# Kernel optimization log

Measured on AMD Instinct MI355X. Metric: run time of the kernel, lower is better.

Reference implementation:

```python
import jax, jax.numpy as jnp
import numpy as np

B, T, C, H = 4, 4096, 512, 64  # batch, seq(patches), n_embed, head_size

def setup_inputs() -> dict:
    key = jax.random.key(0)
    kx, kk, kq, kv = jax.random.split(key, 4)
    x = jax.random.normal(kx, (B, T, C), dtype=jnp.float32)
    # torch nn.Linear(n_embed, head_size).weight is [H, C]; store transposed [C, H]
    Wk = jax.random.normal(kk, (C, H), dtype=jnp.float32) / np.sqrt(C)
    Wq = jax.random.normal(kq, (C, H), dtype=jnp.float32) / np.sqrt(C)
    Wv = jax.random.normal(kv, (C, H), dtype=jnp.float32) / np.sqrt(C)
    return {"x": x, "Wk": Wk, "Wq": Wq, "Wv": Wv}

def reference(x, Wk, Wq, Wv):
    Bn, Tn, Cn = x.shape
    k = x @ Wk  # [B,T,H]
    q = x @ Wq
    v = x @ Wv
    # NOTE: original scales by C**-0.5 with C = n_embed (input dim), not head_size
    scores = jnp.einsum('bth,bsh->bts', q, k) * (Cn ** -0.5)  # [B,T,T]
    causal = jnp.tril(jnp.ones((Tn, Tn), dtype=bool))
    scores = jnp.where(causal, scores, -jnp.inf)
    attn = jax.nn.softmax(scores, axis=-1)
    return jnp.einsum('bts,bsh->bth', attn, v)  # [B,T,H]
```

## Files before the change

### kernel.cpp

```cpp
#include <hip/hip_runtime.h>
#include <hip/hip_bf16.h>

#define Bb 4
#define Tt 4096

typedef __bf16 bf16;
typedef __attribute__((ext_vector_type(8))) __bf16 bf16x8;
typedef __attribute__((ext_vector_type(4))) __bf16 bf16x4;
typedef __attribute__((ext_vector_type(4))) float f32x4;


__global__ __launch_bounds__(256) void wt_kernel(const float* __restrict__ Wk,
                                                 const float* __restrict__ Wq,
                                                 const float* __restrict__ Wv,
                                                 bf16* __restrict__ wt) {
  int idx = blockIdx.x * 256 + threadIdx.x;
  int mat = idx >> 15;
  int rem = idx & 32767;
  int n = rem >> 9;
  int k = rem & 511;
  const float* W = (mat == 0) ? Wk : (mat == 1) ? Wq : Wv;
  float v = W[k * 64 + n];
  if (mat == 1) v *= 0.044194173824159216f;
  wt[idx] = (bf16)v;
}

__global__ __launch_bounds__(256) void proj_kernel(const float* __restrict__ x,
                                                   const bf16* __restrict__ wt,
                                                   bf16* __restrict__ Kb,
                                                   bf16* __restrict__ Qb,
                                                   bf16* __restrict__ VTb) {
  __shared__ __attribute__((aligned(16))) bf16 xs[16][520];
  int tid = threadIdx.x;
  int row0 = blockIdx.x * 16;

  int sr = tid >> 4, sc = (tid & 15) * 4;
  const float* xr = x + (size_t)(row0 + sr) * 512;
#pragma unroll
  for (int j = 0; j < 8; ++j) {
    f32x4 a = *(const f32x4*)(xr + sc + j * 64);
    bf16x4 h;
#pragma unroll
    for (int e = 0; e < 4; ++e) h[e] = (bf16)a[e];
    *(bf16x4*)&xs[sr][sc + j * 64] = h;
  }
  __syncthreads();

  int wave = tid >> 6, lane = tid & 63, m = lane & 15, quad = lane >> 4;
  f32x4 acc[3];
#pragma unroll
  for (int i = 0; i < 3; ++i) acc[i] = (f32x4){0.f, 0.f, 0.f, 0.f};

#pragma unroll 4
  for (int kk = 0; kk < 512; kk += 32) {
    bf16x8 af = *(const bf16x8*)&xs[m][kk + quad * 8];
#pragma unroll
    for (int i = 0; i < 3; ++i) {
      int nt = wave * 3 + i;
      bf16x8 bfr = *(const bf16x8*)(wt + (nt >> 2) * 32768 +
                                    (((nt & 3) * 16) + m) * 512 + kk + quad * 8);
      acc[i] = __builtin_amdgcn_mfma_f32_16x16x32_bf16(af, bfr, acc[i], 0, 0, 0);
    }
  }

  int b = row0 >> 12, tloc = row0 & 4095;
#pragma unroll
  for (int i = 0; i < 3; ++i) {
    int nt = wave * 3 + i, mat = nt >> 2, n0 = (nt & 3) * 16;
    if (mat == 2) {
      bf16x4 pv;
#pragma unroll
      for (int r = 0; r < 4; ++r) pv[r] = (bf16)acc[i][r];
      *(bf16x4*)&VTb[((size_t)b * 64 + n0 + m) * 4096 + tloc + quad * 4] = pv;
    } else {
      bf16* dst = (mat == 0) ? Kb : Qb;
#pragma unroll
      for (int r = 0; r < 4; ++r)
        dst[(size_t)(row0 + quad * 4 + r) * 64 + n0 + m] = (bf16)acc[i][r];
    }
  }
}

__global__ __launch_bounds__(256) void attn_kernel(const bf16* __restrict__ Qb,
                                                   const bf16* __restrict__ Kb,
                                                   const bf16* __restrict__ VTb,
                                                   bf16* __restrict__ Opart,
                                                   float* __restrict__ Lpart,
                                                   float* __restrict__ out) {
  __shared__ __attribute__((aligned(16))) bf16 Kt[64][72];
  __shared__ __attribute__((aligned(16))) bf16 Vt[64][72];
  __shared__ __attribute__((aligned(16))) bf16 Pl[4][16][72];

  int tid = threadIdx.x, wave = tid >> 6, lane = tid & 63;
  int m = lane & 15, quad = lane >> 4, kq = quad * 8;

  int uu = 1151 - (int)blockIdx.x;
  int b = uu / 288, u2 = uu % 288;
  int g = 0;
  while (u2 >= 4 * (g + 1) * (g + 2)) ++g;
  int rr = u2 - 4 * g * (g + 1);
  int qi = 8 * g + rr / (g + 1);
  int c = rr % (g + 1);
  int t0 = qi * 64;
  int s_beg = c * 512;
  int s_end = min(s_beg + 512, t0 + 64);
  int niter = (s_end - s_beg) >> 6;

  const bf16* Qp = Qb + ((size_t)b * Tt + t0 + wave * 16 + m) * 64;
  bf16x8 aq0 = *(const bf16x8*)(Qp + kq);
  bf16x8 aq1 = *(const bf16x8*)(Qp + 32 + kq);

  bf16x8 onesb;
#pragma unroll
  for (int j = 0; j < 8; ++j) onesb[j] = (bf16)1.0f;

  f32x4 o[4];
#pragma unroll
  for (int i = 0; i < 4; ++i) o[i] = (f32x4){0.f, 0.f, 0.f, 0.f};
  f32x4 lsum = (f32x4){0.f, 0.f, 0.f, 0.f};

  int r_ = tid >> 2, seg = tid & 3;
  const bf16* Kbase = Kb + (size_t)b * Tt * 64;
  const bf16* VTbase = VTb + (size_t)b * 64 * 4096;

  const bf16* ks = Kbase + (size_t)(s_beg + r_) * 64 + seg * 16;
  bf16x8 k0 = *(const bf16x8*)ks;
  bf16x8 k1 = *(const bf16x8*)(ks + 8);
  const bf16* vs = VTbase + (size_t)r_ * 4096 + s_beg + seg * 16;
  bf16x8 v0 = *(const bf16x8*)vs;
  bf16x8 v1 = *(const bf16x8*)(vs + 8);

  for (int i = 0; i < niter; ++i) {
    int s0 = s_beg + i * 64;
    __syncthreads();
    *(bf16x8*)&Kt[r_][seg * 16] = k0;
    *(bf16x8*)&Kt[r_][seg * 16 + 8] = k1;
    *(bf16x8*)&Vt[r_][seg * 16] = v0;
    *(bf16x8*)&Vt[r_][seg * 16 + 8] = v1;
    __syncthreads();
    if (i + 1 < niter) {
      int sn = s0 + 64;
      const bf16* ks2 = Kbase + (size_t)(sn + r_) * 64 + seg * 16;
      k0 = *(const bf16x8*)ks2;
      k1 = *(const bf16x8*)(ks2 + 8);
      const bf16* vs2 = VTbase + (size_t)r_ * 4096 + sn + seg * 16;
      v0 = *(const bf16x8*)vs2;
      v1 = *(const bf16x8*)(vs2 + 8);
    }

    f32x4 s[4];
#pragma unroll
    for (int nt = 0; nt < 4; ++nt) {
      bf16x8 b0 = *(const bf16x8*)&Kt[nt * 16 + m][kq];
      bf16x8 b1 = *(const bf16x8*)&Kt[nt * 16 + m][32 + kq];
      f32x4 sa = (f32x4){0.f, 0.f, 0.f, 0.f};
      sa = __builtin_amdgcn_mfma_f32_16x16x32_bf16(aq0, b0, sa, 0, 0, 0);
      sa = __builtin_amdgcn_mfma_f32_16x16x32_bf16(aq1, b1, sa, 0, 0, 0);
      s[nt] = sa;
    }

    if (s0 + 64 > t0) {
#pragma unroll
      for (int nt = 0; nt < 4; ++nt) {
        int col = s0 + nt * 16 + m;
#pragma unroll
        for (int r = 0; r < 4; ++r) {
          int row = t0 + wave * 16 + quad * 4 + r;
          if (col > row) s[nt][r] = -1e30f;
        }
      }
    }

#pragma unroll
    for (int nt = 0; nt < 4; ++nt)
#pragma unroll
      for (int r = 0; r < 4; ++r)
        Pl[wave][quad * 4 + r][nt * 16 + m] = (bf16)__expf(s[nt][r]);

#pragma unroll
    for (int ch = 0; ch < 2; ++ch) {
      bf16x8 ap = *(const bf16x8*)&Pl[wave][m][ch * 32 + kq];
      lsum = __builtin_amdgcn_mfma_f32_16x16x32_bf16(ap, onesb, lsum, 0, 0, 0);
#pragma unroll
      for (int nt = 0; nt < 4; ++nt) {
        bf16x8 bv = *(const bf16x8*)&Vt[nt * 16 + m][ch * 32 + kq];
        o[nt] = __builtin_amdgcn_mfma_f32_16x16x32_bf16(ap, bv, o[nt], 0, 0, 0);
      }
    }
  }

  int rl0 = wave * 16 + quad * 4;
  if (qi < 8) {
    float* op = out + ((size_t)b * Tt + t0) * 64;
#pragma unroll
    for (int r = 0; r < 4; ++r) {
      float inv = 1.0f / lsum[r];
#pragma unroll
      for (int nt = 0; nt < 4; ++nt)
        op[(size_t)(rl0 + r) * 64 + nt * 16 + m] = o[nt][r] * inv;
    }
  } else {
    int p = b * 288 + 4 * g * (g + 1) + (qi - 8 * g) * (g + 1) + c;
    bf16* Op = Opart + (size_t)p * 4096;
#pragma unroll
    for (int r = 0; r < 4; ++r)
#pragma unroll
      for (int nt = 0; nt < 4; ++nt)
        Op[(rl0 + r) * 64 + nt * 16 + m] = (bf16)o[nt][r];
    if (m == 0) {
#pragma unroll
      for (int r = 0; r < 4; ++r) Lpart[p * 64 + rl0 + r] = lsum[r];
    }
  }
}

__global__ __launch_bounds__(256) void combine_kernel(const bf16* __restrict__ Opart,
                                                      const float* __restrict__ Lpart,
                                                      float* __restrict__ out) {
  int blk = blockIdx.x;
  int b = blk / 224, rem = blk % 224;
  int qi = 8 + (rem >> 2), rq = rem & 3;
  int g = qi >> 3, nc = g + 1;
  int pb = b * 288 + 4 * g * (g + 1) + (qi - 8 * g) * (g + 1);
  int t = threadIdx.x, col = t & 63, rl = t >> 6;
#pragma unroll
  for (int rr = 0; rr < 4; ++rr) {
    int row64 = rq * 16 + rl * 4 + rr;
    float L = 0.f, acc = 0.f;
    for (int cc = 0; cc < nc; ++cc) {
      L += Lpart[(pb + cc) * 64 + row64];
      acc += (float)Opart[(size_t)(pb + cc) * 4096 + row64 * 64 + col];
    }
    out[((size_t)b * Tt + qi * 64 + row64) * 64 + col] = acc / L;
  }
}

extern "C" void kernel_launch(void* const* d_in, const int* in_sizes, int n_in,
                              void* d_out, int out_size, void* d_ws, size_t ws_size,
                              hipStream_t stream) {
  const float* x = (const float*)d_in[0];
  const float* Wk = (const float*)d_in[1];
  const float* Wq = (const float*)d_in[2];
  const float* Wv = (const float*)d_in[3];
  float* out = (float*)d_out;

  char* w = (char*)d_ws;
  bf16* wt = (bf16*)w;
  bf16* Kb = (bf16*)(w + 196608);
  bf16* Qb = (bf16*)(w + 2293760);
  bf16* VTb = (bf16*)(w + 4390912);
  bf16* Opart = (bf16*)(w + 6488064);
  float* Lpart = (float*)(w + 15925248);

  wt_kernel<<<384, 256, 0, stream>>>(Wk, Wq, Wv, wt);
  proj_kernel<<<1024, 256, 0, stream>>>(x, wt, Kb, Qb, VTb);
  attn_kernel<<<1152, 256, 0, stream>>>(Qb, Kb, VTb, Opart, Lpart, out);
  combine_kernel<<<896, 256, 0, stream>>>(Opart, Lpart, out);
}
```

Baseline: 137.0 us.

## Keep P in registers via permlane swap, double-buffer K/V, use exp2

Computes S transposed (K as the A operand) so each lane holds probabilities that permlane16_swap can rearrange into the MFMA A-operand layout. This removes the per-wave LDS round trip for P. K/V tiles are double-buffered in shared memory, leaving one barrier per iteration instead of two, and exp is replaced by hardware exp2 with log2(e) folded into the Q scale. Occupancy is hinted with launch_bounds(256,4). The costs are more LDS per block and a more intricate column permutation when indexing V.

```diff
diff --git a/kernel.cpp b/kernel.cpp
--- a/kernel.cpp
+++ b/kernel.cpp
@@ -7,7 +7,10 @@
 typedef __bf16 bf16;
 typedef __attribute__((ext_vector_type(8))) __bf16 bf16x8;
 typedef __attribute__((ext_vector_type(4))) __bf16 bf16x4;
+typedef __attribute__((ext_vector_type(2))) __bf16 bf16x2;
 typedef __attribute__((ext_vector_type(4))) float f32x4;
+typedef __attribute__((ext_vector_type(2))) unsigned int u32x2;
+typedef __attribute__((ext_vector_type(4))) unsigned int u32x4;
 
 
 __global__ __launch_bounds__(256) void wt_kernel(const float* __restrict__ Wk,
@@ -21,7 +24,7 @@
   int k = rem & 511;
   const float* W = (mat == 0) ? Wk : (mat == 1) ? Wq : Wv;
   float v = W[k * 64 + n];
-  if (mat == 1) v *= 0.044194173824159216f;
+  if (mat == 1) v *= 0.0637587165f;
   wt[idx] = (bf16)v;
 }
 
@@ -81,15 +84,26 @@
   }
 }
 
-__global__ __launch_bounds__(256) void attn_kernel(const bf16* __restrict__ Qb,
-                                                   const bf16* __restrict__ Kb,
-                                                   const bf16* __restrict__ VTb,
-                                                   bf16* __restrict__ Opart,
-                                                   float* __restrict__ Lpart,
-                                                   float* __restrict__ out) {
-  __shared__ __attribute__((aligned(16))) bf16 Kt[64][72];
-  __shared__ __attribute__((aligned(16))) bf16 Vt[64][72];
-  __shared__ __attribute__((aligned(16))) bf16 Pl[4][16][72];
+static __device__ inline unsigned pk2(float lo, float hi) {
+  bf16x2 t;
+  t[0] = (bf16)lo;
+  t[1] = (bf16)hi;
+  return __builtin_bit_cast(unsigned int, t);
+}
+static __device__ inline void plswap(unsigned& a, unsigned& b) {
+  u32x2 r = __builtin_amdgcn_permlane16_swap(a, b, false, false);
+  a = r.x;
+  b = r.y;
+}
+
+__global__ __launch_bounds__(256, 4) void attn_kernel(const bf16* __restrict__ Qb,
+                                                      const bf16* __restrict__ Kb,
+                                                      const bf16* __restrict__ VTb,
+                                                      bf16* __restrict__ Opart,
+                                                      float* __restrict__ Lpart,
+                                                      float* __restrict__ out) {
+  __shared__ __attribute__((aligned(16))) bf16 Kt[2][64][72];
+  __shared__ __attribute__((aligned(16))) bf16 Vt[2][64][72];
 
   int tid = threadIdx.x, wave = tid >> 6, lane = tid & 63;
   int m = lane & 15, quad = lane >> 4, kq = quad * 8;
@@ -123,22 +137,29 @@
   const bf16* Kbase = Kb + (size_t)b * Tt * 64;
   const bf16* VTbase = VTb + (size_t)b * 64 * 4096;
 
-  const bf16* ks = Kbase + (size_t)(s_beg + r_) * 64 + seg * 16;
-  bf16x8 k0 = *(const bf16x8*)ks;
-  bf16x8 k1 = *(const bf16x8*)(ks + 8);
-  const bf16* vs = VTbase + (size_t)r_ * 4096 + s_beg + seg * 16;
-  bf16x8 v0 = *(const bf16x8*)vs;
-  bf16x8 v1 = *(const bf16x8*)(vs + 8);
+  {
+    const bf16* ks = Kbase + (size_t)(s_beg + r_) * 64 + seg * 16;
+    bf16x8 k0 = *(const bf16x8*)ks;
+    bf16x8 k1 = *(const bf16x8*)(ks + 8);
+    const bf16* vs = VTbase + (size_t)r_ * 4096 + s_beg + seg * 16;
+    bf16x8 v0 = *(const bf16x8*)vs;
+    bf16x8 v1 = *(const bf16x8*)(vs + 8);
+    *(bf16x8*)&Kt[0][r_][seg * 16] = k0;
+    *(bf16x8*)&Kt[0][r_][seg * 16 + 8] = k1;
+    *(bf16x8*)&Vt[0][r_][seg * 16] = v0;
+    *(bf16x8*)&Vt[0][r_][seg * 16 + 8] = v1;
+  }
+  __syncthreads();
+
+  int qrow = t0 + wave * 16 + m;
 
   for (int i = 0; i < niter; ++i) {
     int s0 = s_beg + i * 64;
-    __syncthreads();
-    *(bf16x8*)&Kt[r_][seg * 16] = k0;
-    *(bf16x8*)&Kt[r_][seg * 16 + 8] = k1;
-    *(bf16x8*)&Vt[r_][seg * 16] = v0;
-    *(bf16x8*)&Vt[r_][seg * 16 + 8] = v1;
-    __syncthreads();
-    if (i + 1 < niter) {
+    int cb = i & 1;
+    bool more = (i + 1 < niter);
+
+    bf16x8 k0, k1, v0, v1;
+    if (more) {
       int sn = s0 + 64;
       const bf16* ks2 = Kbase + (size_t)(sn + r_) * 64 + seg * 16;
       k0 = *(const bf16x8*)ks2;
@@ -151,41 +172,58 @@
     f32x4 s[4];
 #pragma unroll
     for (int nt = 0; nt < 4; ++nt) {
-      bf16x8 b0 = *(const bf16x8*)&Kt[nt * 16 + m][kq];
-      bf16x8 b1 = *(const bf16x8*)&Kt[nt * 16 + m][32 + kq];
+      bf16x8 ak0 = *(const bf16x8*)&Kt[cb][nt * 16 + m][kq];
+      bf16x8 ak1 = *(const bf16x8*)&Kt[cb][nt * 16 + m][32 + kq];
       f32x4 sa = (f32x4){0.f, 0.f, 0.f, 0.f};
-      sa = __builtin_amdgcn_mfma_f32_16x16x32_bf16(aq0, b0, sa, 0, 0, 0);
-      sa = __builtin_amdgcn_mfma_f32_16x16x32_bf16(aq1, b1, sa, 0, 0, 0);
+      sa = __builtin_amdgcn_mfma_f32_16x16x32_bf16(ak0, aq0, sa, 0, 0, 0);
+      sa = __builtin_amdgcn_mfma_f32_16x16x32_bf16(ak1, aq1, sa, 0, 0, 0);
       s[nt] = sa;
     }
 
     if (s0 + 64 > t0) {
+      int kvb = s0 + 4 * quad;
+#pragma unroll
+      for (int nt = 0; nt < 4; ++nt)
+#pragma unroll
+        for (int r = 0; r < 4; ++r)
+          if (kvb + nt * 16 + r > qrow) s[nt][r] = -1e30f;
+    }
+
+    unsigned pA[4], pB[4];
+#pragma unroll
+    for (int nt = 0; nt < 4; ++nt) {
+      float e0 = __builtin_amdgcn_exp2f(s[nt][0]);
+      float e1 = __builtin_amdgcn_exp2f(s[nt][1]);
+      float e2 = __builtin_amdgcn_exp2f(s[nt][2]);
+      float e3 = __builtin_amdgcn_exp2f(s[nt][3]);
+      pA[nt] = pk2(e0, e1);
+      pB[nt] = pk2(e2, e3);
+    }
+
+#pragma unroll
+    for (int ch = 0; ch < 2; ++ch) {
+      unsigned a0 = pA[2 * ch], a1 = pA[2 * ch + 1];
+      unsigned c0 = pB[2 * ch], c1 = pB[2 * ch + 1];
+      plswap(a0, a1);
+      plswap(c0, c1);
+      u32x4 uap = {a0, c0, a1, c1};
+      bf16x8 ap = __builtin_bit_cast(bf16x8, uap);
+      lsum = __builtin_amdgcn_mfma_f32_16x16x32_bf16(ap, onesb, lsum, 0, 0, 0);
+      int fb8 = (4 * ch + 2 * (quad & 1) + (quad >> 1)) * 8;
 #pragma unroll
       for (int nt = 0; nt < 4; ++nt) {
-        int col = s0 + nt * 16 + m;
-#pragma unroll
-        for (int r = 0; r < 4; ++r) {
-          int row = t0 + wave * 16 + quad * 4 + r;
-          if (col > row) s[nt][r] = -1e30f;
-        }
-      }
-    }
-
-#pragma unroll
-    for (int nt = 0; nt < 4; ++nt)
-#pragma unroll
-      for (int r = 0; r < 4; ++r)
-        Pl[wave][quad * 4 + r][nt * 16 + m] = (bf16)__expf(s[nt][r]);
-
-#pragma unroll
-    for (int ch = 0; ch < 2; ++ch) {
-      bf16x8 ap = *(const bf16x8*)&Pl[wave][m][ch * 32 + kq];
-      lsum = __builtin_amdgcn_mfma_f32_16x16x32_bf16(ap, onesb, lsum, 0, 0, 0);
-#pragma unroll
-      for (int nt = 0; nt < 4; ++nt) {
-        bf16x8 bv = *(const bf16x8*)&Vt[nt * 16 + m][ch * 32 + kq];
+        bf16x8 bv = *(const bf16x8*)&Vt[cb][nt * 16 + m][fb8];
         o[nt] = __builtin_amdgcn_mfma_f32_16x16x32_bf16(ap, bv, o[nt], 0, 0, 0);
       }
+    }
+
+    if (more) {
+      int nb = cb ^ 1;
+      *(bf16x8*)&Kt[nb][r_][seg * 16] = k0;
+      *(bf16x8*)&Kt[nb][r_][seg * 16 + 8] = k1;
+      *(bf16x8*)&Vt[nb][r_][seg * 16] = v0;
+      *(bf16x8*)&Vt[nb][r_][seg * 16 + 8] = v1;
+      __syncthreads();
     }
   }
 
```

After: 134.4 us. No clear change (-1.9%).
